# Kernel tuning notes

Measured on AMD Instinct MI355X. Metric: run time of the kernel, lower is better.

Reference implementation:

```python
import jax, jax.numpy as jnp
import numpy as np

B, L = 128, 256          # trees per batch, leaves per tree (perfect binary tree)
V, D, H = 50000, 300, 512  # vocab, word_dim, tree_input_dim == output_dim


def setup_inputs() -> dict:
    key = jax.random.key(0)
    ks = jax.random.split(key, 6)
    token_ids = jax.random.randint(ks[0], (B, L), 0, V)
    scale_e = np.sqrt(3.0 / D).astype(np.float32)  # reset_embedding uniform(-scale, scale)
    emb_table = jax.random.uniform(ks[1], (V, D), jnp.float32, -scale_e, scale_e)
    s = 0.02
    Wx = jax.random.normal(ks[2], (D, 5 * H), jnp.float32) * s  # leaf input -> (i, fl, fr, o, u)
    Ul = jax.random.normal(ks[3], (H, 5 * H), jnp.float32) * s  # left child h
    Ur = jax.random.normal(ks[4], (H, 5 * H), jnp.float32) * s  # right child h
    b = jax.random.normal(ks[5], (5 * H,), jnp.float32) * s
    return {"token_ids": token_ids, "emb_table": emb_table, "Wx": Wx, "Ul": Ul, "Ur": Ur, "b": b}


def _cell(xproj, hl, hr, cl, cr, Ul, Ur, b):
    # Binary tree-LSTM cell (Tai et al., fold-style) with per-child forget gates.
    g = xproj + hl @ Ul + hr @ Ur + b            # [..., 5H]
    i, fl, fr, o, u = jnp.split(g, 5, axis=-1)
    c = jax.nn.sigmoid(i) * jnp.tanh(u) + jax.nn.sigmoid(fl) * cl + jax.nn.sigmoid(fr) * cr
    h = jax.nn.sigmoid(o) * jnp.tanh(c)
    return h, c


def reference(token_ids, emb_table, Wx, Ul, Ur, b):
    # Eval mode: all dropouts are identity.
    x = emb_table[token_ids]                      # [B, L, D] leaf word embeddings
    z = jnp.zeros((B, L, H), x.dtype)             # leaf children states are zero
    h, c = _cell(x @ Wx, z, z, z, z, Ul, Ur, b)   # all leaves at once
    hs = [h]
    # Level-wise bottom-up over the perfect binary tree (internal nodes: inputs=None).
    while h.shape[1] > 1:
        hl, hr = h[:, 0::2], h[:, 1::2]
        cl, cr = c[:, 0::2], c[:, 1::2]
        h, c = _cell(jnp.float32(0.0), hl, hr, cl, cr, Ul, Ur, b)
        hs.append(h)
    # Collected hidden states of all 2L-1 nodes (leaves first, then levels up to root).
    return jnp.concatenate(hs, axis=1)            # [B, 2L-1, H]
```

## Files before the change

### kernel.cpp

```cpp
#include <hip/hip_runtime.h>
#include <hip/hip_bf16.h>
#include <cstdint>

#define BB 128
#define LL 256
#define DD 300
#define HH 512
#define TOUT 511
#define NGATE 2560

typedef __attribute__((ext_vector_type(8))) short bf16x8;
typedef __attribute__((ext_vector_type(4))) float f32x4;

__device__ __forceinline__ float rcpf(float x){ return __builtin_amdgcn_rcpf(x); }
__device__ __forceinline__ float ex2f(float x){ return __builtin_amdgcn_exp2f(x); }
__device__ __forceinline__ float sigf(float x){ return rcpf(1.0f + ex2f(x * -1.44269504f)); }
__device__ __forceinline__ float tanh_fast(float x){ return 1.0f - 2.0f*rcpf(ex2f(x * 2.88539008f) + 1.0f); }

__device__ __forceinline__ void load_lds16(const void* g, void* l) {
  __builtin_amdgcn_global_load_lds(
      (const __attribute__((address_space(1))) unsigned int*)g,
      (__attribute__((address_space(3))) unsigned int*)l, 16, 0, 0);
}

#define VMWAIT(n) asm volatile("s_waitcnt vmcnt(" #n ")" ::: "memory")

__global__ __launch_bounds__(256) void transpose_cvt(const float* __restrict__ src,
    __hip_bfloat16* __restrict__ dst, int Ksrc, int Kdst, int koff)
{
  __shared__ float t[64][65];
  const int tid = threadIdx.x;
  const int k0 = blockIdx.x * 64;
  const int n0 = blockIdx.y * 64;
  #pragma unroll
  for (int p = 0; p < 16; ++p) {
    int lin = p*256 + tid;
    int ki = lin >> 6, nj = lin & 63;
    t[ki][nj] = (k0 + ki < Ksrc) ? src[(size_t)(k0+ki)*NGATE + n0 + nj] : 0.f;
  }
  __syncthreads();
  #pragma unroll
  for (int p = 0; p < 16; ++p) {
    int lin = p*256 + tid;
    int ni = lin >> 6, kj = lin & 63;
    dst[(size_t)(n0+ni)*Kdst + koff + k0 + kj] = __float2bfloat16(t[kj][ni]);
  }
}

__global__ void embed_cvt(const int* __restrict__ tok, const float* __restrict__ emb,
                          __hip_bfloat16* __restrict__ A0)
{
  int k = blockIdx.x * 64 + threadIdx.x;
  int r = blockIdx.y * 4 + threadIdx.y;
  int tk = tok[r];
  float v = (k < DD) ? emb[(size_t)tk*DD + k] : 0.f;
  A0[(size_t)r*320 + k] = __float2bfloat16(v);
}

__global__ __launch_bounds__(512, 4) void gemm_cell(
    const __hip_bfloat16* __restrict__ A, const __hip_bfloat16* __restrict__ Wt,
    int K, const float* __restrict__ bias, const float* __restrict__ cprev,
    float* __restrict__ out, __hip_bfloat16* __restrict__ hout, float* __restrict__ cout,
    int lkshift, int sc, int numM)
{
  constexpr int BUFS = 28672;
  __shared__ __align__(16) char lds[2*BUFS];

  const int tid  = threadIdx.x;
  const int lane = tid & 63;
  const int wid  = tid >> 6;
  const int wm   = wid >> 2;
  const int wn   = wid & 3;
  const int bid  = blockIdx.x;
  int m, s;
  if (numM >= 8) { m = (bid & 7) + ((bid >> 6) << 3); s = (bid >> 3) & 7; }
  else           { m = bid % numM;  s = bid / numM; }
  const int r0   = m * 128;
  const int n0   = s * 64;
  const size_t rowK = (size_t)K * 2;

  const char* gsrc[4];
  int gi0 = (wid < 4) ? wid*4 : 16 + (wid-4)*3;
  #pragma unroll
  for (int i = 0; i < 4; ++i) {
    int gi = gi0 + i;
    int row = (gi < 8) ? gi*16 + (lane >> 2) : (gi-8)*16 + (lane >> 2);
    int cg = (lane & 3) ^ ((row >> 1) & 3);
    if (gi < 8) {
      gsrc[i] = (const char*)A + (size_t)(r0 + row)*rowK + cg*16;
    } else {
      int grow = (row >> 6)*512 + n0 + (row & 63);
      gsrc[i] = (const char*)Wt + (size_t)grow*rowK + cg*16;
    }
  }
  const int ldst0 = gi0*1024 + lane*16;

  f32x4 acc[4][5];
  #pragma unroll
  for (int mf = 0; mf < 4; ++mf)
    #pragma unroll
    for (int g5 = 0; g5 < 5; ++g5)
      acc[mf][g5] = (f32x4){0.f,0.f,0.f,0.f};

  const int nk = K >> 5;
  auto stage = [&](int buf, int kt){
    char* base = lds + buf*BUFS + ldst0;
    const size_t kb = (size_t)kt*64;
    if (wid < 4) {
      #pragma unroll
      for (int i = 0; i < 4; ++i) load_lds16(gsrc[i] + kb, base + i*1024);
    } else {
      #pragma unroll
      for (int i = 0; i < 3; ++i) load_lds16(gsrc[i] + kb, base + i*1024);
    }
  };

  stage(0, 0);
  int cur = 0;
  for (int kt = 0; kt < nk; ++kt) {
    if (kt + 1 < nk) {
      stage(cur ^ 1, kt + 1);
      if (wid < 4) VMWAIT(4); else VMWAIT(3);
    } else {
      VMWAIT(0);
    }
    __builtin_amdgcn_s_barrier();

    const char* Ab = lds + cur*BUFS;
    const char* Bb = Ab + 8192;
    const int q = lane >> 4;
    bf16x8 b[5];
    #pragma unroll
    for (int g5 = 0; g5 < 5; ++g5) {
      int c = g5*64 + wn*16 + (lane & 15);
      b[g5] = *(const bf16x8*)(Bb + c*64 + ((q ^ ((c >> 1) & 3))*16));
    }
    __builtin_amdgcn_s_setprio(1);
    #pragma unroll
    for (int mf = 0; mf < 4; ++mf) {
      int r = wm*64 + mf*16 + (lane & 15);
      bf16x8 av = *(const bf16x8*)(Ab + r*64 + ((q ^ ((r >> 1) & 3))*16));
      #pragma unroll
      for (int g5 = 0; g5 < 5; ++g5)
        acc[mf][g5] = __builtin_amdgcn_mfma_f32_16x16x32_bf16(av, b[g5], acc[mf][g5], 0, 0, 0);
    }
    __builtin_amdgcn_s_setprio(0);
    __builtin_amdgcn_s_barrier();
    cur ^= 1;
  }

  const int Lmask = (1 << lkshift) - 1;
  const int jg = n0 + wn*16 + (lane & 15);
  float bia[5];
  #pragma unroll
  for (int g5 = 0; g5 < 5; ++g5) bia[g5] = bias[g5*HH + jg];
  #pragma unroll
  for (int mf = 0; mf < 4; ++mf) {
    #pragma unroll
    for (int v = 0; v < 4; ++v) {
      int rr = r0 + wm*64 + mf*16 + (lane >> 4)*4 + v;
      float gi  = acc[mf][0][v] + bia[0];
      float gfl = acc[mf][1][v] + bia[1];
      float gfr = acc[mf][2][v] + bia[2];
      float go  = acc[mf][3][v] + bia[3];
      float gu  = acc[mf][4][v] + bia[4];
      float cl = 0.f, cr = 0.f;
      if (cprev) {
        cl = cprev[(size_t)(2*rr)*HH + jg];
        cr = cprev[(size_t)(2*rr)*HH + HH + jg];
      }
      float cc = sigf(gi)*tanh_fast(gu) + sigf(gfl)*cl + sigf(gfr)*cr;
      float hh = sigf(go)*tanh_fast(cc);
      int b = rr >> lkshift;
      int t = rr & Lmask;
      out[((size_t)b*TOUT + sc + t)*HH + jg] = hh;
      hout[(size_t)rr*HH + jg] = __float2bfloat16(hh);
      cout[(size_t)rr*HH + jg] = cc;
    }
  }
}

extern "C" void kernel_launch(void* const* d_in, const int* in_sizes, int n_in,
                              void* d_out, int out_size, void* d_ws, size_t ws_size,
                              hipStream_t stream) {
  (void)in_sizes; (void)n_in; (void)out_size; (void)ws_size;
  const int*   tok  = (const int*)d_in[0];
  const float* emb  = (const float*)d_in[1];
  const float* Wx   = (const float*)d_in[2];
  const float* Ul   = (const float*)d_in[3];
  const float* Ur   = (const float*)d_in[4];
  const float* bias = (const float*)d_in[5];
  float* out = (float*)d_out;

  char* ws = (char*)d_ws;
  size_t off = 0;
  __hip_bfloat16* Wb0t = (__hip_bfloat16*)(ws + off); off += (size_t)NGATE*320*2;
  __hip_bfloat16* Wb1t = (__hip_bfloat16*)(ws + off); off += (size_t)NGATE*1024*2;
  __hip_bfloat16* hA   = (__hip_bfloat16*)(ws + off); off += (size_t)32768*HH*2;
  __hip_bfloat16* hB   = (__hip_bfloat16*)(ws + off); off += (size_t)16384*HH*2;
  float*          cA   = (float*)(ws + off);          off += (size_t)32768*HH*4;
  float*          cB   = (float*)(ws + off);          off += (size_t)16384*HH*4;
  __hip_bfloat16* A0   = (__hip_bfloat16*)cB;

  transpose_cvt<<<dim3(5, 40), 256, 0, stream>>>(Wx, Wb0t, DD, 320, 0);
  transpose_cvt<<<dim3(8, 40), 256, 0, stream>>>(Ul, Wb1t, HH, 1024, 0);
  transpose_cvt<<<dim3(8, 40), 256, 0, stream>>>(Ur, Wb1t, HH, 1024, 512);
  embed_cvt<<<dim3(5, 8192), dim3(64,4), 0, stream>>>(tok, emb, A0);

  gemm_cell<<<(32768/128)*8, 512, 0, stream>>>(A0, Wb0t, 320, bias, nullptr,
                                               out, hA, cA, 8, 0, 32768/128);
  for (int k = 1; k <= 8; ++k) {
    int M = 32768 >> k;
    int sc = HH - (HH >> k);
    const __hip_bfloat16* Ain = (k & 1) ? hA : hB;
    __hip_bfloat16*       hO  = (k & 1) ? hB : hA;
    const float*          cI  = (k & 1) ? cA : cB;
    float*                cO  = (k & 1) ? cB : cA;
    int numM = M / 128;
    gemm_cell<<<numM*8, 512, 0, stream>>>(Ain, Wb1t, 1024, bias, cI,
                                          out, hO, cO, 8 - k, sc, numM);
  }
}
```

Before: 468.4 us.

## Add 256-row GEMM-cell kernel reading A from global for large levels

Adds a gemm_big kernel that uses 256-row by 64x5-column tiles with 64-wide K steps for the leaf level and the larger internal levels (M >= 8192). Only the weight tile is staged in LDS through async global-to-LDS loads. Each wave reads its A fragments straight from global memory into registers, with 8x5 MFMA accumulators per wave. The aim is to reuse each staged B tile across more rows and halve the barrier count per K, at the cost of higher register pressure (occupancy 2) and uncached A reads that may stall the MFMA stream.

```diff
diff --git a/kernel.cpp b/kernel.cpp
--- a/kernel.cpp
+++ b/kernel.cpp
@@ -55,6 +55,121 @@
   int tk = tok[r];
   float v = (k < DD) ? emb[(size_t)tk*DD + k] : 0.f;
   A0[(size_t)r*320 + k] = __float2bfloat16(v);
+}
+
+__global__ __launch_bounds__(512, 2) void gemm_big(
+    const __hip_bfloat16* __restrict__ A, const __hip_bfloat16* __restrict__ Wt,
+    int K, const float* __restrict__ bias, const float* __restrict__ cprev,
+    float* __restrict__ out, __hip_bfloat16* __restrict__ hout, float* __restrict__ cout,
+    int lkshift, int sc)
+{
+  constexpr int BUFS = 40960;
+  __shared__ __align__(16) char lds[2*BUFS];
+
+  const int tid  = threadIdx.x;
+  const int lane = tid & 63;
+  const int wid  = tid >> 6;
+  const int wm   = wid >> 2;
+  const int wn   = wid & 3;
+  const int bid  = blockIdx.x;
+  const int m    = (bid & 7) + ((bid >> 6) << 3);
+  const int s    = (bid >> 3) & 7;
+  const int r0   = m * 256;
+  const int n0   = s * 64;
+  const size_t rowK = (size_t)K * 2;
+
+  unsigned boff[5];
+  #pragma unroll
+  for (int i = 0; i < 5; ++i) {
+    int gi = wid*5 + i;
+    int c  = gi*8 + (lane >> 3);
+    int kc = (lane & 7) ^ ((lane >> 3) & 7);
+    int grow = (c >> 6)*512 + n0 + (c & 63);
+    boff[i] = (unsigned)((size_t)grow*rowK) + kc*16;
+  }
+  const int ldst0 = (wid*5)*1024 + lane*16;
+
+  const unsigned aoff0 = (unsigned)((size_t)(r0 + wm*128 + (lane & 15))*rowK) + (lane >> 4)*16;
+  const unsigned mfstride = (unsigned)(rowK * 16);
+
+  f32x4 acc[8][5];
+  #pragma unroll
+  for (int mf = 0; mf < 8; ++mf)
+    #pragma unroll
+    for (int g5 = 0; g5 < 5; ++g5)
+      acc[mf][g5] = (f32x4){0.f,0.f,0.f,0.f};
+
+  const int nt = K >> 6;
+  auto stage = [&](int buf, int t){
+    char* base = lds + buf*BUFS + ldst0;
+    const unsigned kb = (unsigned)t*128;
+    #pragma unroll
+    for (int i = 0; i < 5; ++i)
+      load_lds16((const char*)Wt + boff[i] + kb, base + i*1024);
+  };
+
+  stage(0, 0);
+  int cur = 0;
+  for (int t = 0; t < nt; ++t) {
+    if (t == 0) VMWAIT(0); else VMWAIT(5);
+    __builtin_amdgcn_s_barrier();
+    if (t + 1 < nt) stage(cur ^ 1, t + 1);
+    __builtin_amdgcn_sched_barrier(0);
+
+    const char* Bb = lds + cur*BUFS;
+    #pragma unroll
+    for (int ks = 0; ks < 2; ++ks) {
+      const char* ab = (const char*)A + aoff0 + (unsigned)t*128 + ks*64;
+      bf16x8 a[8], b[5];
+      #pragma unroll
+      for (int mf = 0; mf < 8; ++mf)
+        a[mf] = *(const bf16x8*)(ab + mf*mfstride);
+      #pragma unroll
+      for (int g5 = 0; g5 < 5; ++g5) {
+        int c = g5*64 + wn*16 + (lane & 15);
+        int q = (ks*4 + (lane >> 4)) ^ (c & 7);
+        b[g5] = *(const bf16x8*)(Bb + c*128 + q*16);
+      }
+      __builtin_amdgcn_s_setprio(1);
+      #pragma unroll
+      for (int mf = 0; mf < 8; ++mf)
+        #pragma unroll
+        for (int g5 = 0; g5 < 5; ++g5)
+          acc[mf][g5] = __builtin_amdgcn_mfma_f32_16x16x32_bf16(a[mf], b[g5], acc[mf][g5], 0, 0, 0);
+      __builtin_amdgcn_s_setprio(0);
+    }
+    cur ^= 1;
+  }
+
+  const int Lmask = (1 << lkshift) - 1;
+  const int jg = n0 + wn*16 + (lane & 15);
+  float bia[5];
+  #pragma unroll
+  for (int g5 = 0; g5 < 5; ++g5) bia[g5] = bias[g5*HH + jg];
+  #pragma unroll
+  for (int mf = 0; mf < 8; ++mf) {
+    #pragma unroll
+    for (int v = 0; v < 4; ++v) {
+      int rr = r0 + wm*128 + mf*16 + (lane >> 4)*4 + v;
+      float gi  = acc[mf][0][v] + bia[0];
+      float gfl = acc[mf][1][v] + bia[1];
+      float gfr = acc[mf][2][v] + bia[2];
+      float go  = acc[mf][3][v] + bia[3];
+      float gu  = acc[mf][4][v] + bia[4];
+      float cl = 0.f, cr = 0.f;
+      if (cprev) {
+        cl = cprev[(size_t)(2*rr)*HH + jg];
+        cr = cprev[(size_t)(2*rr)*HH + HH + jg];
+      }
+      float cc = sigf(gi)*tanh_fast(gu) + sigf(gfl)*cl + sigf(gfr)*cr;
+      float hh = sigf(go)*tanh_fast(cc);
+      int b = rr >> lkshift;
+      int t = rr & Lmask;
+      out[((size_t)b*TOUT + sc + t)*HH + jg] = hh;
+      hout[(size_t)rr*HH + jg] = __float2bfloat16(hh);
+      cout[(size_t)rr*HH + jg] = cc;
+    }
+  }
 }
 
 __global__ __launch_bounds__(512, 4) void gemm_cell(
@@ -207,8 +322,8 @@
   transpose_cvt<<<dim3(8, 40), 256, 0, stream>>>(Ur, Wb1t, HH, 1024, 512);
   embed_cvt<<<dim3(5, 8192), dim3(64,4), 0, stream>>>(tok, emb, A0);
 
-  gemm_cell<<<(32768/128)*8, 512, 0, stream>>>(A0, Wb0t, 320, bias, nullptr,
-                                               out, hA, cA, 8, 0, 32768/128);
+  gemm_big<<<(32768/256)*8, 512, 0, stream>>>(A0, Wb0t, 320, bias, nullptr,
+                                              out, hA, cA, 8, 0);
   for (int k = 1; k <= 8; ++k) {
     int M = 32768 >> k;
     int sc = HH - (HH >> k);
@@ -216,8 +331,13 @@
     __hip_bfloat16*       hO  = (k & 1) ? hB : hA;
     const float*          cI  = (k & 1) ? cA : cB;
     float*                cO  = (k & 1) ? cB : cA;
-    int numM = M / 128;
-    gemm_cell<<<numM*8, 512, 0, stream>>>(Ain, Wb1t, 1024, bias, cI,
-                                          out, hO, cO, 8 - k, sc, numM);
-  }
-}
+    if (M >= 8192) {
+      gemm_big<<<(M/256)*8, 512, 0, stream>>>(Ain, Wb1t, 1024, bias, cI,
+                                              out, hO, cO, 8 - k, sc);
+    } else {
+      int numM = M / 128;
+      gemm_cell<<<numM*8, 512, 0, stream>>>(Ain, Wb1t, 1024, bias, cI,
+                                            out, hO, cO, 8 - k, sc, numM);
+    }
+  }
+}
```

Measured after the change: 636.0 us. +35.8%, slower.
